# Performance work log

Measured on AMD Instinct MI355X. Metric: run time of the kernel, lower is better.

## Reference

```python
import jax, jax.numpy as jnp
import numpy as np


def setup_inputs() -> dict:
    key = jax.random.key(0)
    x = jax.random.normal(key, (8, 2048, 3), dtype=jnp.float32)
    return {"x": x, "k": 16}


def reference(x, k):
    b, n, d = x.shape
    xf = x.reshape(b * n, d)                      # flatten across batch, as in the torch module
    sq = jnp.sum(xf * xf, axis=1, keepdims=True)  # [BN, 1]
    pair = 2.0 * (xf @ xf.T) - sq - sq.T          # [BN, BN] = -dist^2
    # torch topk(largest=False) on pair == largest of (-pair) == largest squared distance
    neg_vals, idx = jax.lax.top_k(-pair, k + 1)   # [BN, k+1]
    dists = -neg_vals
    dists = dists[:, 1:].reshape(b, n, k)
    idx = idx[:, 1:].reshape(b, n, k)
    return dists, idx
```

## Files before the change

kernel.cpp:

```cpp
#include <hip/hip_runtime.h>
#include <stdint.h>

#define BN       16384
#define NTILES   256
#define NB       64
#define KOUT     16
#define MARGIN   0.01f

typedef float v2f __attribute__((ext_vector_type(2)));
union F4 { float4 f4; v2f p[2]; float f[4]; };

#define WS_TAB    0
#define WS_IDX    (WS_TAB + BN * 16)
#define WS_BND    (WS_IDX + BN * 4)
#define WS_HIST   (WS_BND + NTILES * 8)
#define WS_HMAX   (WS_HIST + 64 * NB * 4)

__device__ __forceinline__ unsigned key_u(unsigned u) {
    return u ^ ((unsigned)((int)u >> 31) | 0x80000000u);
}
__device__ __forceinline__ unsigned wshr1(unsigned v, unsigned oldv) {
    return (unsigned)__builtin_amdgcn_update_dpp((int)oldv, (int)v, 0x138 ,
                                                 0xF, 0xF, false);
}
__device__ __forceinline__ double wror1_f64(double v) {
    const unsigned long long u = (unsigned long long)__double_as_longlong(v);
    unsigned lo = (unsigned)u, hi = (unsigned)(u >> 32);
    lo = (unsigned)__builtin_amdgcn_update_dpp((int)lo, (int)lo, 0x13C, 0xF, 0xF, false);
    hi = (unsigned)__builtin_amdgcn_update_dpp((int)hi, (int)hi, 0x13C, 0xF, 0xF, false);
    return __longlong_as_double((long long)(((unsigned long long)hi << 32) | lo));
}
#define RL16(T) __uint_as_float((unsigned)__builtin_amdgcn_readlane(__float_as_int(T), 16))

__device__ __forceinline__ float sq_of(float gx, float gy, float gz) {
    return __fadd_rn(__fadd_rn(__fmul_rn(gx, gx), __fmul_rn(gy, gy)), __fmul_rn(gz, gz));
}
__device__ __forceinline__ int bucket_of(float sq) {
    const float rho = __fsqrt_rn(sq);
    int b = (int)(64.0f * (1.0f - rho * 0.2f));
    return (b < 0) ? 0 : ((b > 63) ? 63 : b);
}

#define DRAIN(m, p, jvec, T, J)                                                     \
    while (m) {                                                                     \
        const int b_ = (int)__builtin_ctzll(m);                                     \
        m &= m - 1;                                                                 \
        const float pc_ = __uint_as_float(                                          \
            (unsigned)__builtin_amdgcn_readlane(__float_as_int(p), b_));            \
        const unsigned jc_ = (unsigned)__builtin_amdgcn_readlane((int)(jvec), b_);  \
        const float Tup_ =                                                          \
            __uint_as_float(wshr1(__float_as_uint(T), 0xFF800000u ));       \
        const unsigned Jup_ = wshr1((J), 0u);                                       \
        const bool lt_ = (pc_ < Tup_) || ((pc_ == Tup_) && (jc_ < Jup_));           \
        const float Tn_ = lt_ ? Tup_ : pc_;                                         \
        const unsigned Jn_ = lt_ ? Jup_ : jc_;                                      \
        const bool sel_ = (pc_ < (T)) || ((pc_ == (T)) && (jc_ < (J)));             \
        (T) = sel_ ? Tn_ : (T);                                                     \
        (J) = sel_ ? Jn_ : (J);                                                     \
    }

#define EVALC(c, d2)                                                                \
    asm("v_pk_mul_f32 %0, %1, %2 op_sel:[0,0] op_sel_hi:[0,1]"                      \
        : "=v"(d2) : "v"((c).p[0]), "v"(c0A));                                      \
    asm("v_pk_fma_f32 %0, %1, %2, %0 op_sel:[1,0,0] op_sel_hi:[1,1,1]"              \
        : "+v"(d2) : "v"((c).p[0]), "v"(c1A));                                      \
    asm("v_pk_fma_f32 %0, %1, %2, %0 op_sel:[0,0,0] op_sel_hi:[0,1,1]"              \
        : "+v"(d2) : "v"((c).p[1]), "v"(c2A));                                      \
    asm("v_pk_add_f32 %0, %0, %1" : "+v"(d2) : "v"(nsq01));                         \
    asm("v_pk_add_f32 %0, %0, %1 op_sel:[0,1] op_sel_hi:[1,1]"                      \
        : "+v"(d2) : "v"((c).p[1]));

#define TILE_AT(t)                                                                  \
    F4 c; c.f4 = tab[(t) * 64 + lane];                                              \
    const unsigned jvec = idxarr[(t) * 64 + lane];                                  \
    v2f d2; EVALC(c, d2)

#define PROCESS_LOADED()                                                            \
    do {                                                                            \
        uint64_t m0 = __ballot(d2[0] <= fF0);                                       \
        uint64_t m1 = __ballot(d2[1] <= fF1);                                       \
        if (m0 | m1) {                                                              \
            const float p0 = d2[0], p1 = d2[1];                                     \
            DRAIN(m0, p0, jvec, T0, J0)                                             \
            DRAIN(m1, p1, jvec, T1, J1)                                             \
            fF0 = RL16(T0); thr0 = __fsub_rn(-fF0, MARGIN);                         \
            fF1 = RL16(T1); thr1 = __fsub_rn(-fF1, MARGIN);                         \
        }                                                                           \
    } while (0)

__device__ __forceinline__ void presort64(float p, unsigned j, int lane, double* sw,
                                          float& T, unsigned& J) {
    const double dm = (double)key_u(__float_as_uint(p)) * 16384.0 + (double)j;
    double rot = dm;
    unsigned rank = 0;
#pragma unroll
    for (int s = 0; s < 63; ++s) {
        rot = wror1_f64(rot);
        rank += (rot < dm) ? 1u : 0u;
    }
    sw[rank] = __longlong_as_double(
        (long long)(((unsigned long long)j << 32) | __float_as_uint(p)));
    const unsigned long long v = (unsigned long long)__double_as_longlong(sw[lane]);
    T = __uint_as_float((unsigned)(v & 0xFFFFFFFFull));
    J = (unsigned)(v >> 32);
}

__global__ __launch_bounds__(256) void k_hist(const float* __restrict__ x,
                                              unsigned* __restrict__ hist,
                                              unsigned* __restrict__ hmax) {
    __shared__ unsigned h[NB], m[NB];
    const int tid = threadIdx.x;
    if (tid < NB) { h[tid] = 0u; m[tid] = 0u; }
    __syncthreads();
    const int i = blockIdx.x * 256 + tid;
    const float sq = sq_of(x[3 * i], x[3 * i + 1], x[3 * i + 2]);
    const int b = bucket_of(sq);
    atomicAdd(&h[b], 1u);
    atomicMax(&m[b], __float_as_uint(sq));
    __syncthreads();
    if (tid < NB) {
        hist[blockIdx.x * NB + tid] = h[tid];
        hmax[blockIdx.x * NB + tid] = m[tid];
    }
}

__global__ __launch_bounds__(256) void k_scatter(const float* __restrict__ x,
                                                 const unsigned* __restrict__ hist,
                                                 const unsigned* __restrict__ hmax,
                                                 float4* __restrict__ tab,
                                                 unsigned* __restrict__ idxarr,
                                                 float2* __restrict__ bnd) {
    __shared__ unsigned tot_s[NB], pre_s[NB], basev[NB + 1], c[NB], sfx[NB];
    const int tid = threadIdx.x;
    const int g0 = (int)blockIdx.x;
    if (tid < NB) {
        unsigned s = 0, pre = 0;
        for (int g = 0; g < 64; ++g) {
            const unsigned hh = hist[g * NB + tid];
            pre += (g < g0) ? hh : 0u;
            s += hh;
        }
        tot_s[tid] = s;
        pre_s[tid] = pre;
        if (g0 == 0) {
            unsigned mx = 0;
            for (int g = 0; g < 64; ++g) {
                const unsigned w = hmax[g * NB + tid];
                mx = (w > mx) ? w : mx;
            }
            sfx[tid] = mx;
        }
    }
    __syncthreads();
    if (tid == 0) {
        unsigned s = 0;
        for (int b = 0; b < NB; ++b) { basev[b] = s; s += tot_s[b]; }
        basev[NB] = s;
        if (g0 == 0) {
            unsigned M = 0;
            for (int b = NB - 1; b >= 0; --b) {
                const unsigned w = sfx[b]; M = (w > M) ? w : M; sfx[b] = M;
            }
        }
    }
    __syncthreads();
    if (tid < NB) c[tid] = basev[tid] + pre_s[tid];
    __syncthreads();
    const int i = g0 * 256 + tid;
    const float gx = x[3 * i], gy = x[3 * i + 1], gz = x[3 * i + 2];
    const float sq = sq_of(gx, gy, gz);
    const int b = bucket_of(sq);
    const unsigned pos = atomicAdd(&c[b], 1u);
    tab[pos] = make_float4(gx, gy, gz, -sq);
    idxarr[pos] = (unsigned)i;
    if (g0 == 0) {
        const unsigned posn = (unsigned)tid * 64u;
        int b2 = 0;
        for (int bb = 0; bb < NB; ++bb) b2 = (basev[bb] <= posn) ? bb : b2;
        const float B = __uint_as_float(sfx[b2]);
        const float sqB_up = __uint_as_float(__float_as_uint(__fsqrt_rn(B)) + 2u);
        bnd[tid] = make_float2(B, sqB_up);
    }
}

__global__ __launch_bounds__(256) void knn_far_kernel(
    const float* __restrict__ x, const float4* __restrict__ tab,
    const unsigned* __restrict__ idxarr, const float2* __restrict__ bnd,
    float* __restrict__ out_d, float* __restrict__ out_i) {
    __shared__ double swall[4 * 64];
    const int tid  = threadIdx.x;
    const int lane = tid & 63;
    const int wid  = tid >> 6;
    double* sw = swall + wid * 64;
    const int q0 = (blockIdx.x * 4 + wid) * 2;
    const int q1 = q0 + 1;

    const float a0 = x[3 * q0], a1 = x[3 * q0 + 1], a2 = x[3 * q0 + 2];
    const float b0 = x[3 * q1], b1 = x[3 * q1 + 1], b2 = x[3 * q1 + 2];
    const float sq0 = sq_of(a0, a1, a2), sq1 = sq_of(b0, b1, b2);
    const v2f nsq01 = {-sq0, -sq1};
    const v2f c0A = {2.0f * a0, 2.0f * b0};
    const v2f c1A = {2.0f * a1, 2.0f * b1};
    const v2f c2A = {2.0f * a2, 2.0f * b2};
    const float twor0 = 2.0f * __uint_as_float(__float_as_uint(__fsqrt_rn(sq0)) + 2u);
    const float twor1 = 2.0f * __uint_as_float(__float_as_uint(__fsqrt_rn(sq1)) + 2u);

    float T0, T1; unsigned J0, J1;
    float fF0, fF1, thr0, thr1;

    {
        TILE_AT(0)
        presort64(d2[0], jvec, lane, sw, T0, J0);
        presort64(d2[1], jvec, lane, sw, T1, J1);
        fF0 = RL16(T0); thr0 = __fsub_rn(-fF0, MARGIN);
        fF1 = RL16(T1); thr1 = __fsub_rn(-fF1, MARGIN);
    }
#pragma unroll
    for (int t = 1; t < 4; ++t) {
        TILE_AT(t)
        PROCESS_LOADED();
    }
    for (int t = 4; t < NTILES; ++t) {
        const float2 bd = bnd[t];
        const float u0 = __builtin_fmaf(twor0, bd.y, __fadd_rn(sq0, bd.x));
        const float u1 = __builtin_fmaf(twor1, bd.y, __fadd_rn(sq1, bd.x));
        if (u0 < thr0 && u1 < thr1) break;
        TILE_AT(t)
        PROCESS_LOADED();
    }

    if (lane >= 1 && lane <= KOUT) {
        const int r = lane - 1;
        out_d[q0 * KOUT + r] = T0;
        out_i[q0 * KOUT + r] = (float)J0;
        out_d[q1 * KOUT + r] = T1;
        out_i[q1 * KOUT + r] = (float)J1;
    }
}

extern "C" void kernel_launch(void* const* d_in, const int* in_sizes, int n_in,
                              void* d_out, int out_size, void* d_ws, size_t ws_size,
                              hipStream_t stream) {
    const float* x = (const float*)d_in[0];
    char* ws = (char*)d_ws;
    float4*   tab    = (float4*)(ws + WS_TAB);
    unsigned* idxarr = (unsigned*)(ws + WS_IDX);
    float2*   bnd    = (float2*)(ws + WS_BND);
    unsigned* hist   = (unsigned*)(ws + WS_HIST);
    unsigned* hmax   = (unsigned*)(ws + WS_HMAX);
    float* out_d = (float*)d_out;
    float* out_i = out_d + (size_t)BN * KOUT;

    hipLaunchKernelGGL(k_hist,    dim3(64), dim3(256), 0, stream, x, hist, hmax);
    hipLaunchKernelGGL(k_scatter, dim3(64), dim3(256), 0, stream, x, hist, hmax,
                       tab, idxarr, bnd);
    hipLaunchKernelGGL(knn_far_kernel, dim3(BN / 8), dim3(256), 0, stream,
                       x, tab, idxarr, bnd, out_d, out_i);
}
```

Before: 83.18 us.

## Fuse histogram and scatter kernels using an in-kernel grid barrier

Measured after the change: 90.76 us. +9.1%, slower.

```diff
diff --git a/kernel.cpp b/kernel.cpp
--- a/kernel.cpp
+++ b/kernel.cpp
@@ -6,6 +6,7 @@
 #define NB       64
 #define KOUT     16
 #define MARGIN   0.01f
+#define MAGIC    0x5EEDF00Du
 
 typedef float v2f __attribute__((ext_vector_type(2)));
 union F4 { float4 f4; v2f p[2]; float f[4]; };
@@ -15,6 +16,7 @@
 #define WS_BND    (WS_IDX + BN * 4)
 #define WS_HIST   (WS_BND + NTILES * 8)
 #define WS_HMAX   (WS_HIST + 64 * NB * 4)
+#define WS_FLAGS  (WS_HMAX + 64 * NB * 4)
 
 __device__ __forceinline__ unsigned key_u(unsigned u) {
     return u ^ ((unsigned)((int)u >> 31) | 0x80000000u);
@@ -105,34 +107,43 @@
     J = (unsigned)(v >> 32);
 }
 
-__global__ __launch_bounds__(256) void k_hist(const float* __restrict__ x,
-                                              unsigned* __restrict__ hist,
-                                              unsigned* __restrict__ hmax) {
+__global__ __launch_bounds__(256) void k_prep64(const float* __restrict__ x,
+                                                unsigned* __restrict__ hist,
+                                                unsigned* __restrict__ hmax,
+                                                unsigned* __restrict__ flags,
+                                                float4* __restrict__ tab,
+                                                unsigned* __restrict__ idxarr,
+                                                float2* __restrict__ bnd) {
     __shared__ unsigned h[NB], m[NB];
+    __shared__ unsigned tot_s[NB], pre_s[NB], basev[NB + 1], c[NB], sfx[NB];
     const int tid = threadIdx.x;
+    const int g0  = (int)blockIdx.x;
+
     if (tid < NB) { h[tid] = 0u; m[tid] = 0u; }
     __syncthreads();
-    const int i = blockIdx.x * 256 + tid;
-    const float sq = sq_of(x[3 * i], x[3 * i + 1], x[3 * i + 2]);
+    const int i = g0 * 256 + tid;
+    const float gx = x[3 * i], gy = x[3 * i + 1], gz = x[3 * i + 2];
+    const float sq = sq_of(gx, gy, gz);
     const int b = bucket_of(sq);
     atomicAdd(&h[b], 1u);
     atomicMax(&m[b], __float_as_uint(sq));
     __syncthreads();
     if (tid < NB) {
-        hist[blockIdx.x * NB + tid] = h[tid];
-        hmax[blockIdx.x * NB + tid] = m[tid];
-    }
-}
-
-__global__ __launch_bounds__(256) void k_scatter(const float* __restrict__ x,
-                                                 const unsigned* __restrict__ hist,
-                                                 const unsigned* __restrict__ hmax,
-                                                 float4* __restrict__ tab,
-                                                 unsigned* __restrict__ idxarr,
-                                                 float2* __restrict__ bnd) {
-    __shared__ unsigned tot_s[NB], pre_s[NB], basev[NB + 1], c[NB], sfx[NB];
-    const int tid = threadIdx.x;
-    const int g0 = (int)blockIdx.x;
+        hist[g0 * NB + tid] = h[tid];
+        hmax[g0 * NB + tid] = m[tid];
+    }
+    __syncthreads();
+    if (tid == 0) {
+        __threadfence();
+        __hip_atomic_store(&flags[g0], MAGIC, __ATOMIC_RELEASE, __HIP_MEMORY_SCOPE_AGENT);
+    }
+    if (tid < 64) {
+        while (__hip_atomic_load(&flags[tid], __ATOMIC_ACQUIRE,
+                                 __HIP_MEMORY_SCOPE_AGENT) != MAGIC) {}
+    }
+    __syncthreads();
+    __threadfence();
+
     if (tid < NB) {
         unsigned s = 0, pre = 0;
         for (int g = 0; g < 64; ++g) {
@@ -154,22 +165,18 @@
     __syncthreads();
     if (tid == 0) {
         unsigned s = 0;
-        for (int b = 0; b < NB; ++b) { basev[b] = s; s += tot_s[b]; }
+        for (int bb = 0; bb < NB; ++bb) { basev[bb] = s; s += tot_s[bb]; }
         basev[NB] = s;
         if (g0 == 0) {
             unsigned M = 0;
-            for (int b = NB - 1; b >= 0; --b) {
-                const unsigned w = sfx[b]; M = (w > M) ? w : M; sfx[b] = M;
+            for (int bb = NB - 1; bb >= 0; --bb) {
+                const unsigned w = sfx[bb]; M = (w > M) ? w : M; sfx[bb] = M;
             }
         }
     }
     __syncthreads();
     if (tid < NB) c[tid] = basev[tid] + pre_s[tid];
     __syncthreads();
-    const int i = g0 * 256 + tid;
-    const float gx = x[3 * i], gy = x[3 * i + 1], gz = x[3 * i + 2];
-    const float sq = sq_of(gx, gy, gz);
-    const int b = bucket_of(sq);
     const unsigned pos = atomicAdd(&c[b], 1u);
     tab[pos] = make_float4(gx, gy, gz, -sq);
     idxarr[pos] = (unsigned)i;
@@ -248,11 +255,11 @@
     float2*   bnd    = (float2*)(ws + WS_BND);
     unsigned* hist   = (unsigned*)(ws + WS_HIST);
     unsigned* hmax   = (unsigned*)(ws + WS_HMAX);
+    unsigned* flags  = (unsigned*)(ws + WS_FLAGS);
     float* out_d = (float*)d_out;
     float* out_i = out_d + (size_t)BN * KOUT;
 
-    hipLaunchKernelGGL(k_hist,    dim3(64), dim3(256), 0, stream, x, hist, hmax);
-    hipLaunchKernelGGL(k_scatter, dim3(64), dim3(256), 0, stream, x, hist, hmax,
+    hipLaunchKernelGGL(k_prep64, dim3(64), dim3(256), 0, stream, x, hist, hmax, flags,
                        tab, idxarr, bnd);
     hipLaunchKernelGGL(knn_far_kernel, dim3(BN / 8), dim3(256), 0, stream,
                        x, tab, idxarr, bnd, out_d, out_i);
```
